# Performance work log

Hardware: AMD Instinct MI355X
Metric: run time of the kernel (lower is better)

The kernel has to match this reference:

```python
import jax, jax.numpy as jnp
import numpy as np

B, T, C = 2, 2048, 1024
NH = 16
DFF = 4096
EPS = 1e-5


def setup_inputs() -> dict:
    key = jax.random.key(0)
    ks = jax.random.split(key, 12)
    s = 0.02
    return {
        "x": jax.random.normal(ks[0], (B, T, C), dtype=jnp.float32),
        "Wq": jax.random.normal(ks[1], (C, C), dtype=jnp.float32) * s,
        "bq": jax.random.normal(ks[2], (C,), dtype=jnp.float32) * s,
        "Wk": jax.random.normal(ks[3], (C, C), dtype=jnp.float32) * s,
        "bk": jax.random.normal(ks[4], (C,), dtype=jnp.float32) * s,
        "Wv": jax.random.normal(ks[5], (C, C), dtype=jnp.float32) * s,
        "bv": jax.random.normal(ks[6], (C,), dtype=jnp.float32) * s,
        "W1": jax.random.normal(ks[7], (C, DFF), dtype=jnp.float32) * s,
        "b1": jax.random.normal(ks[8], (DFF,), dtype=jnp.float32) * s,
        "W2": jax.random.normal(ks[9], (DFF, C), dtype=jnp.float32) * s,
        "b2": jax.random.normal(ks[10], (C,), dtype=jnp.float32) * s,
        "ln_w": jnp.ones((C,), dtype=jnp.float32),
    }


def _layernorm(x, w):
    # LayerNorm over last dim, weight only (bias=False), eps=1e-5
    mu = jnp.mean(x, axis=-1, keepdims=True)
    var = jnp.mean(jnp.square(x - mu), axis=-1, keepdims=True)
    return (x - mu) / jnp.sqrt(var + EPS) * w


def reference(x, Wq, bq, Wk, bk, Wv, bv, W1, b1, W2, b2, ln_w):
    Bx, Tx, Cx = x.shape
    hd = Cx // NH
    q = (x @ Wq + bq).reshape(Bx, Tx, NH, hd).transpose(0, 2, 1, 3)  # [B,H,T,hd]
    k = (x @ Wk + bk).reshape(Bx, Tx, NH, hd).transpose(0, 2, 1, 3)
    v = (x @ Wv + bv).reshape(Bx, Tx, NH, hd).transpose(0, 2, 1, 3)
    # NOTE: original scales by sqrt(d_k) = sqrt(FULL model dim C), not head dim
    scores = jnp.einsum("bhqd,bhkd->bhqk", q, k) / jnp.sqrt(jnp.float32(Cx))
    causal = jnp.tril(jnp.ones((Tx, Tx), dtype=bool))
    scores = jnp.where(causal[None, None, :, :], scores, -jnp.inf)
    attn = jax.nn.softmax(scores, axis=-1)
    head_out = jnp.einsum("bhqk,bhkd->bhqd", attn, v)
    a = head_out.transpose(0, 2, 1, 3).reshape(Bx, Tx, Cx)
    # residuals: out = x + ln(x) with SHARED ln weight
    h = a + _layernorm(a, ln_w)
    f = jax.nn.relu(h @ W1 + b1) @ W2 + b2
    out = f + _layernorm(f, ln_w)
    return out
```

## Files before the change

kernel.cpp:

```cpp
#include <hip/hip_runtime.h>
#include <math.h>


typedef __attribute__((ext_vector_type(8))) short short8;
typedef __attribute__((ext_vector_type(4))) float f32x4;

__device__ __forceinline__ unsigned short f2bf(float f) {
    unsigned u = __builtin_bit_cast(unsigned, f);
    unsigned r = u + 0x7fffu + ((u >> 16) & 1u);
    return (unsigned short)(r >> 16);
}

__global__ __launch_bounds__(256) void prep_kernel(
    const float* __restrict__ x,  const float* __restrict__ Wq,
    const float* __restrict__ Wk, const float* __restrict__ Wv,
    const float* __restrict__ W1, const float* __restrict__ W2,
    const float* __restrict__ bq, const float* __restrict__ bk,
    unsigned short* __restrict__ x_bf,  unsigned short* __restrict__ Wqk_t,
    unsigned short* __restrict__ Wvt,   unsigned short* __restrict__ W1t,
    unsigned short* __restrict__ W2t,   float* __restrict__ bqk)
{
    const int bid = blockIdx.x;
    const int tid = threadIdx.x;

    if (bid < 4096) {
        const int i = (bid * 256 + tid) * 4;
        float4 v = *(const float4*)(x + i);
        ushort4 o;
        o.x = f2bf(v.x); o.y = f2bf(v.y); o.z = f2bf(v.z); o.w = f2bf(v.w);
        *(ushort4*)(x_bf + i) = o;
        return;
    }
    if (bid >= 15360) {
        const int i = (bid - 15360) * 256 + tid;
        bqk[i] = i < 1024 ? bq[i] : bk[i - 1024];
        return;
    }

    __shared__ float tile[32][33];
    const float* src; unsigned short* dst; int K, N, t;
    if (bid < 5120)       { t = bid - 4096;  src = Wq; dst = Wqk_t;            K = 1024; N = 1024; }
    else if (bid < 6144)  { t = bid - 5120;  src = Wk; dst = Wqk_t + 1048576;  K = 1024; N = 1024; }
    else if (bid < 7168)  { t = bid - 6144;  src = Wv; dst = Wvt;              K = 1024; N = 1024; }
    else if (bid < 11264) { t = bid - 7168;  src = W1; dst = W1t;              K = 1024; N = 4096; }
    else                  { t = bid - 11264; src = W2; dst = W2t;              K = 4096; N = 1024; }

    const int ncols = N >> 5;
    const int n0 = (t % ncols) * 32;
    const int k0 = (t / ncols) * 32;
    const int tx = tid & 31;
    const int ty = tid >> 5;
#pragma unroll
    for (int i = 0; i < 4; ++i)
        tile[ty + i * 8][tx] = src[(size_t)(k0 + ty + i * 8) * N + n0 + tx];
    __syncthreads();
#pragma unroll
    for (int i = 0; i < 4; ++i)
        dst[(size_t)(n0 + ty + i * 8) * K + k0 + tx] = f2bf(tile[tx][ty + i * 8]);
}

template <int TM, int TN>
__device__ __forceinline__ void gemm_body(
    unsigned short* As, unsigned short* Bs,
    const unsigned short* __restrict__ A, const unsigned short* __restrict__ Bt,
    const float* __restrict__ bias, float* __restrict__ Cf,
    unsigned short* __restrict__ Cb, int M, int N, int K, int mode,
    int bx, int by)
{
    constexpr int NI   = TM / 32;
    constexpr int NJ   = TN / 32;
    constexpr int NPA  = TM / 8;
    constexpr int NPB  = TN / 8;
    constexpr int MAXA = (NPA + 3) / 4;
    constexpr int MAXB = (NPB + 3) / 4;

    const int tid  = threadIdx.x;
    const int lane = tid & 63;
    const int w    = tid >> 6;
    const int wm   = (w & 1) * (TM / 2);
    const int wn   = (w >> 1) * (TN / 2);
    const int fm   = lane & 15;
    const int quad = lane >> 4;

    const int row0 = by * TM;
    const int col0 = bx * TN;

    const int srow = lane >> 3;
    const int scol = ((lane & 7) ^ srow) << 3;

    const unsigned short* aptr[MAXA];
    int aoff[MAXA];
#pragma unroll
    for (int i = 0; i < MAXA; ++i) {
        const int p = w + i * 4;
        if (p < NPA) {
            aptr[i] = A + (size_t)(row0 + p * 8 + srow) * K + scol;
            aoff[i] = p * 8 * 64;
        }
    }
    const unsigned short* bptr[MAXB];
    int boff[MAXB];
#pragma unroll
    for (int i = 0; i < MAXB; ++i) {
        const int p = w + i * 4;
        if (p < NPB) {
            bptr[i] = Bt + (size_t)(col0 + p * 8 + srow) * K + scol;
            boff[i] = p * 8 * 64;
        }
    }

    f32x4 acc[NI][NJ] = {};

    for (int k0 = 0; k0 < K; k0 += 64) {
        __syncthreads();
#pragma unroll
        for (int i = 0; i < MAXA; ++i)
            if (w + i * 4 < NPA)
                __builtin_amdgcn_global_load_lds(
                    (const __attribute__((address_space(1))) void*)(aptr[i] + k0),
                    (__attribute__((address_space(3))) void*)&As[aoff[i]], 16, 0, 0);
#pragma unroll
        for (int i = 0; i < MAXB; ++i)
            if (w + i * 4 < NPB)
                __builtin_amdgcn_global_load_lds(
                    (const __attribute__((address_space(1))) void*)(bptr[i] + k0),
                    (__attribute__((address_space(3))) void*)&Bs[boff[i]], 16, 0, 0);
        __syncthreads();

#pragma unroll
        for (int kh = 0; kh < 2; ++kh) {
            short8 af[NI], bf[NJ];
#pragma unroll
            for (int i = 0; i < NI; ++i) {
                const int r = wm + i * 16 + fm;
                const int sl = ((kh << 2) | quad) ^ (r & 7);
                af[i] = *(const short8*)&As[r * 64 + sl * 8];
            }
#pragma unroll
            for (int j = 0; j < NJ; ++j) {
                const int r = wn + j * 16 + fm;
                const int sl = ((kh << 2) | quad) ^ (r & 7);
                bf[j] = *(const short8*)&Bs[r * 64 + sl * 8];
            }
#pragma unroll
            for (int i = 0; i < NI; ++i)
#pragma unroll
                for (int j = 0; j < NJ; ++j)
                    acc[i][j] = __builtin_amdgcn_mfma_f32_16x16x32_bf16(
                        af[i], bf[j], acc[i][j], 0, 0, 0);
        }
    }

#pragma unroll
    for (int j = 0; j < NJ; ++j) {
        const int col = col0 + wn + j * 16 + fm;
        const float bcol = (mode == 3) ? 0.f : bias[col];
#pragma unroll
        for (int i = 0; i < NI; ++i) {
            const int rbase = row0 + wm + i * 16 + quad * 4;
#pragma unroll
            for (int r = 0; r < 4; ++r) {
                const int row = rbase + r;
                float val = acc[i][j][r] + ((mode == 3) ? bias[row] : bcol);
                if (mode == 1) val = fmaxf(val, 0.f);
                if (mode == 0) Cf[(size_t)row * N + col] = val;
                else           Cb[(size_t)row * N + col] = f2bf(val);
            }
        }
    }
}

template <int TM, int TN>
__global__ __launch_bounds__(256) void gemm_bf16_mfma(
    const unsigned short* __restrict__ A, const unsigned short* __restrict__ Bt,
    const float* __restrict__ bias, float* __restrict__ Cf,
    unsigned short* __restrict__ Cb, int M, int N, int K, int mode)
{
    __shared__ unsigned short As[TM * 64];
    __shared__ unsigned short Bs[TN * 64];
    gemm_body<TM, TN>(As, Bs, A, Bt, bias, Cf, Cb, M, N, K, mode,
                      blockIdx.x, blockIdx.y);
}

template <int TM, int TN>
__global__ __launch_bounds__(256) void gemm_xcd(
    const unsigned short* __restrict__ A, const unsigned short* __restrict__ Bt,
    const float* __restrict__ bias, float* __restrict__ Cf,
    unsigned short* __restrict__ Cb, int M, int N, int K, int mode,
    int nx, int rows_per_xcd)
{
    __shared__ unsigned short As[TM * 64];
    __shared__ unsigned short Bs[TN * 64];
    const int xcd = blockIdx.x & 7;
    const int idx = blockIdx.x >> 3;
    const int bx  = idx % nx;
    const int by  = xcd * rows_per_xcd + idx / nx;
    gemm_body<TM, TN>(As, Bs, A, Bt, bias, Cf, Cb, M, N, K, mode, bx, by);
}

template <int TM, int TN>
__global__ __launch_bounds__(256) void gemm_dual(
    const unsigned short* __restrict__ A0, const unsigned short* __restrict__ B0,
    const float* __restrict__ bias0, unsigned short* __restrict__ C0,
    int M0, int N0, int K0, int mode0, int nb0, int nx0,
    const unsigned short* __restrict__ A1, const unsigned short* __restrict__ B1,
    const float* __restrict__ bias1, unsigned short* __restrict__ C1,
    int M1, int N1, int K1, int mode1, int nx1)
{
    __shared__ unsigned short As[TM * 64];
    __shared__ unsigned short Bs[TN * 64];
    const int bid = blockIdx.x;
    if (bid < nb0) {
        gemm_body<TM, TN>(As, Bs, A0, B0, bias0, nullptr, C0,
                          M0, N0, K0, mode0, bid % nx0, bid / nx0);
    } else {
        const int t = bid - nb0;
        gemm_body<TM, TN>(As, Bs, A1, B1, bias1, nullptr, C1,
                          M1, N1, K1, mode1, t % nx1, t / nx1);
    }
}

__global__ __launch_bounds__(256) void fattn_mfma(
    const unsigned short* __restrict__ qk,
    const unsigned short* __restrict__ vt,
    float* __restrict__ a)
{
    const int T = 2048, LDQK = 2048, LDVT = 4096, OUTC = 1024;
    const float cs = 0.04508422f;

    __shared__ unsigned short Qs[64 * 64];
    __shared__ unsigned short Ks[64 * 64];
    __shared__ unsigned short Vs[64 * 64];
    __shared__ unsigned short Ps[4][16][72];

    const int tid  = threadIdx.x;
    const int lane = tid & 63;
    const int w    = tid >> 6;
    const int fm   = lane & 15;
    const int quad = lane >> 4;
    const int srow = lane >> 3;
    const int scol = ((lane & 7) ^ srow) << 3;

    const int n  = blockIdx.x;
    const int lo = n & 255, hi = n >> 8;
    const int h  = ((lo >> 5) & 7) | ((hi & 1) << 3);
    const int b  = hi >> 1;
    const int qv = lo & 31;
    const int u  = ((qv & 1) << 4) | ((qv & 2) << 2) | (qv & 4) |
                   ((qv & 8) >> 2) | ((qv & 16) >> 4);
    const int qb = (hi & 1) ? (31 - u) : u;
    const int q0 = qb * 64;

    const size_t rowbase = (size_t)b * T;

#pragma unroll
    for (int i = 0; i < 2; ++i) {
        const int p = w * 2 + i;
        const unsigned short* src = qk + (rowbase + q0 + p * 8 + srow) * LDQK
                                       + h * 64 + scol;
        __builtin_amdgcn_global_load_lds(
            (const __attribute__((address_space(1))) void*)src,
            (__attribute__((address_space(3))) void*)&Qs[p * 8 * 64], 16, 0, 0);
    }
    __syncthreads();
    const int qr = w * 16 + fm;
    short8 qf0 = *(const short8*)&Qs[qr * 64 + ((quad ^ (qr & 7)) << 3)];
    short8 qf1 = *(const short8*)&Qs[qr * 64 + (((4 | quad) ^ (qr & 7)) << 3)];

    short8 ones;
#pragma unroll
    for (int i = 0; i < 8; ++i) ones[i] = (short)0x3F80;

    f32x4 o[4] = {};
    f32x4 lacc = {};

    const int qglob = q0 + w * 16 + fm;

    for (int jt = 0; jt <= qb; ++jt) {
        const int j0 = jt * 64;
        __syncthreads();
#pragma unroll
        for (int i = 0; i < 4; ++i) {
            const int unit = w * 4 + i;
            if (unit < 8) {
                const unsigned short* ksrc = qk + (rowbase + j0 + unit * 8 + srow) * LDQK
                                                + 1024 + h * 64 + scol;
                __builtin_amdgcn_global_load_lds(
                    (const __attribute__((address_space(1))) void*)ksrc,
                    (__attribute__((address_space(3))) void*)&Ks[unit * 8 * 64], 16, 0, 0);
            } else {
                const int p = unit - 8;
                const unsigned short* vsrc = vt + (size_t)(h * 64 + p * 8 + srow) * LDVT
                                                + rowbase + j0 + scol;
                __builtin_amdgcn_global_load_lds(
                    (const __attribute__((address_space(1))) void*)vsrc,
                    (__attribute__((address_space(3))) void*)&Vs[p * 8 * 64], 16, 0, 0);
            }
        }
        __syncthreads();

        f32x4 s[4];
#pragma unroll
        for (int j = 0; j < 4; ++j) {
            const int r = j * 16 + fm;
            short8 k0 = *(const short8*)&Ks[r * 64 + ((quad ^ (r & 7)) << 3)];
            short8 k1 = *(const short8*)&Ks[r * 64 + (((4 | quad) ^ (r & 7)) << 3)];
            f32x4 acc = {};
            acc = __builtin_amdgcn_mfma_f32_16x16x32_bf16(k0, qf0, acc, 0, 0, 0);
            acc = __builtin_amdgcn_mfma_f32_16x16x32_bf16(k1, qf1, acc, 0, 0, 0);
            s[j] = acc;
        }

        if (jt == qb) {
#pragma unroll
            for (int j = 0; j < 4; ++j) {
                const int kbase = j0 + j * 16 + quad * 4;
#pragma unroll
                for (int r = 0; r < 4; ++r) {
                    const float e = exp2f(s[j][r] * cs);
                    s[j][r] = (kbase + r > qglob) ? 0.f : e;
                }
            }
        } else {
#pragma unroll
            for (int j = 0; j < 4; ++j)
#pragma unroll
                for (int r = 0; r < 4; ++r)
                    s[j][r] = exp2f(s[j][r] * cs);
        }

#pragma unroll
        for (int j = 0; j < 4; ++j) {
            const unsigned d0 = (unsigned)f2bf(s[j][0]) | ((unsigned)f2bf(s[j][1]) << 16);
            const unsigned d1 = (unsigned)f2bf(s[j][2]) | ((unsigned)f2bf(s[j][3]) << 16);
            *(uint2*)&Ps[w][fm][j * 16 + quad * 4] = make_uint2(d0, d1);
        }
        short8 pf0 = *(const short8*)&Ps[w][fm][quad * 8];
        short8 pf1 = *(const short8*)&Ps[w][fm][32 + quad * 8];

#pragma unroll
        for (int jd = 0; jd < 4; ++jd) {
            const int r = jd * 16 + fm;
            short8 v0 = *(const short8*)&Vs[r * 64 + ((quad ^ (r & 7)) << 3)];
            short8 v1 = *(const short8*)&Vs[r * 64 + (((4 | quad) ^ (r & 7)) << 3)];
            o[jd] = __builtin_amdgcn_mfma_f32_16x16x32_bf16(pf0, v0, o[jd], 0, 0, 0);
            o[jd] = __builtin_amdgcn_mfma_f32_16x16x32_bf16(pf1, v1, o[jd], 0, 0, 0);
        }
        lacc = __builtin_amdgcn_mfma_f32_16x16x32_bf16(pf0, ones, lacc, 0, 0, 0);
        lacc = __builtin_amdgcn_mfma_f32_16x16x32_bf16(pf1, ones, lacc, 0, 0, 0);
    }

    const size_t orow = rowbase + q0 + w * 16 + quad * 4;
#pragma unroll
    for (int r = 0; r < 4; ++r) {
        const float inv = 1.0f / lacc[r];
#pragma unroll
        for (int jd = 0; jd < 4; ++jd)
            a[(orow + r) * OUTC + h * 64 + jd * 16 + fm] = o[jd][r] * inv;
    }
}

__global__ __launch_bounds__(256) void add_ln_kernel(
    const float* __restrict__ in, const float* __restrict__ w,
    float* __restrict__ outf, unsigned short* __restrict__ outb, int bf16_out)
{
    const int C = 1024;
    const int row = blockIdx.x;
    const int tid = threadIdx.x;
    const int lane = tid & 63;
    const int wv   = tid >> 6;

    __shared__ float red[8];

    float4 xv = *(const float4*)(in + (size_t)row * C + tid * 4);

    float s = xv.x + xv.y + xv.z + xv.w;
#pragma unroll
    for (int o = 32; o > 0; o >>= 1) s += __shfl_xor(s, o, 64);
    if (lane == 0) red[wv] = s;
    __syncthreads();
    const float mu = (red[0] + red[1] + red[2] + red[3]) * (1.0f / 1024.0f);

    float dx = xv.x - mu, dy = xv.y - mu, dz = xv.z - mu, dw = xv.w - mu;
    float v = dx * dx + dy * dy + dz * dz + dw * dw;
#pragma unroll
    for (int o = 32; o > 0; o >>= 1) v += __shfl_xor(v, o, 64);
    if (lane == 0) red[4 + wv] = v;
    __syncthreads();
    const float rstd = rsqrtf((red[4] + red[5] + red[6] + red[7]) * (1.0f / 1024.0f)
                              + 1e-5f);

    float4 wvv = *(const float4*)(w + tid * 4);
    float ox = xv.x + dx * rstd * wvv.x;
    float oy = xv.y + dy * rstd * wvv.y;
    float oz = xv.z + dz * rstd * wvv.z;
    float ow = xv.w + dw * rstd * wvv.w;
    if (bf16_out) {
        ushort4 o4;
        o4.x = f2bf(ox); o4.y = f2bf(oy); o4.z = f2bf(oz); o4.w = f2bf(ow);
        *(ushort4*)(outb + (size_t)row * C + tid * 4) = o4;
    } else {
        *(float4*)(outf + (size_t)row * C + tid * 4) = make_float4(ox, oy, oz, ow);
    }
}

extern "C" void kernel_launch(void* const* d_in, const int* in_sizes, int n_in,
                              void* d_out, int out_size, void* d_ws, size_t ws_size,
                              hipStream_t stream)
{
    const float* x    = (const float*)d_in[0];
    const float* Wq   = (const float*)d_in[1];
    const float* bq   = (const float*)d_in[2];
    const float* Wk   = (const float*)d_in[3];
    const float* bk   = (const float*)d_in[4];
    const float* Wv   = (const float*)d_in[5];
    const float* bv   = (const float*)d_in[6];
    const float* W1   = (const float*)d_in[7];
    const float* b1   = (const float*)d_in[8];
    const float* W2   = (const float*)d_in[9];
    const float* b2   = (const float*)d_in[10];
    const float* ln_w = (const float*)d_in[11];
    float* out = (float*)d_out;
    char* ws = (char*)d_ws;

    const int B = 2, T = 2048, C = 1024, DFF = 4096;
    const int M = B * T;
    const size_t MB = 1048576;

    unsigned short* qk_bf = (unsigned short*)(ws);
    unsigned short* vt_bf = (unsigned short*)(ws + 16 * MB);
    float*          a     = (float*)(ws + 24 * MB);
    unsigned short* x_bf  = (unsigned short*)(ws + 40 * MB);
    unsigned short* Wqk_t = (unsigned short*)(ws + 48 * MB);
    unsigned short* Wvt   = (unsigned short*)(ws + 52 * MB);
    unsigned short* W1t   = (unsigned short*)(ws + 54 * MB);
    unsigned short* W2t   = (unsigned short*)(ws + 62 * MB);
    float*          bqk   = (float*)(ws + 70 * MB);
    unsigned short* u_bf  = (unsigned short*)(ws + 71 * MB);
    unsigned short* h_bf  = x_bf;
    float*          f     = (float*)(ws);

    dim3 blk(256);

    prep_kernel<<<dim3(15368), blk, 0, stream>>>(
        x, Wq, Wk, Wv, W1, W2, bq, bk,
        x_bf, Wqk_t, Wvt, W1t, W2t, bqk);

    gemm_dual<64, 128><<<dim3(1536), blk, 0, stream>>>(
        x_bf, Wqk_t, bqk, qk_bf, M, 2 * C, C, 2, 1024, 16,
        Wvt, x_bf, bv, vt_bf, C, M, C, 3, 32);

    fattn_mfma<<<dim3(1024), blk, 0, stream>>>(qk_bf, vt_bf, a);

    add_ln_kernel<<<dim3(M), blk, 0, stream>>>(a, ln_w, nullptr, h_bf, 1);

    gemm_bf16_mfma<64, 128><<<dim3(DFF / 128, M / 64), blk, 0, stream>>>(
        h_bf, W1t, b1, nullptr, u_bf, M, DFF, C, 1);

    gemm_xcd<128, 64><<<dim3(512), blk, 0, stream>>>(
        u_bf, W2t, b2, f, nullptr, M, C, DFF, 0, 16, 4);

    add_ln_kernel<<<dim3(M), blk, 0, stream>>>(f, ln_w, out, nullptr, 0);
}
```

Before: 316.1 us.

## Split-K the W2 GEMM into two halves and widen prep transpose tiles

The second FFN GEMM (K=4096) now launches 1024 blocks, each computing half the K range. One half writes with bias into f and the other writes a raw partial into the old attention buffer. The final add+LayerNorm kernel sums the two partials as it loads them. This doubles parallelism for a GEMM that previously had only 512 blocks, at the cost of an extra fp32 M×C write and read. Separately, the weight transpose/convert prep kernel uses 64×64 tiles with float4 loads and ushort4 stores, cutting block count and making memory accesses wider.

```diff
diff --git a/kernel.cpp b/kernel.cpp
--- a/kernel.cpp
+++ b/kernel.cpp
@@ -31,32 +31,45 @@
         *(ushort4*)(x_bf + i) = o;
         return;
     }
-    if (bid >= 15360) {
-        const int i = (bid - 15360) * 256 + tid;
+    if (bid >= 6912) {
+        const int i = (bid - 6912) * 256 + tid;
         bqk[i] = i < 1024 ? bq[i] : bk[i - 1024];
         return;
     }
 
-    __shared__ float tile[32][33];
+    __shared__ float tile[64][65];
     const float* src; unsigned short* dst; int K, N, t;
-    if (bid < 5120)       { t = bid - 4096;  src = Wq; dst = Wqk_t;            K = 1024; N = 1024; }
-    else if (bid < 6144)  { t = bid - 5120;  src = Wk; dst = Wqk_t + 1048576;  K = 1024; N = 1024; }
-    else if (bid < 7168)  { t = bid - 6144;  src = Wv; dst = Wvt;              K = 1024; N = 1024; }
-    else if (bid < 11264) { t = bid - 7168;  src = W1; dst = W1t;              K = 1024; N = 4096; }
-    else                  { t = bid - 11264; src = W2; dst = W2t;              K = 4096; N = 1024; }
-
-    const int ncols = N >> 5;
-    const int n0 = (t % ncols) * 32;
-    const int k0 = (t / ncols) * 32;
-    const int tx = tid & 31;
-    const int ty = tid >> 5;
-#pragma unroll
-    for (int i = 0; i < 4; ++i)
-        tile[ty + i * 8][tx] = src[(size_t)(k0 + ty + i * 8) * N + n0 + tx];
+    if (bid < 4352)      { t = bid - 4096; src = Wq; dst = Wqk_t;           K = 1024; N = 1024; }
+    else if (bid < 4608) { t = bid - 4352; src = Wk; dst = Wqk_t + 1048576; K = 1024; N = 1024; }
+    else if (bid < 4864) { t = bid - 4608; src = Wv; dst = Wvt;             K = 1024; N = 1024; }
+    else if (bid < 5888) { t = bid - 4864; src = W1; dst = W1t;             K = 1024; N = 4096; }
+    else                 { t = bid - 5888; src = W2; dst = W2t;             K = 4096; N = 1024; }
+
+    const int ncols = N >> 6;
+    const int n0 = (t % ncols) * 64;
+    const int k0 = (t / ncols) * 64;
+    const int tx = tid & 15;
+    const int ty = tid >> 4;
+#pragma unroll
+    for (int i = 0; i < 4; ++i) {
+        const int r = ty + i * 16;
+        float4 v = *(const float4*)(src + (size_t)(k0 + r) * N + n0 + tx * 4);
+        tile[r][tx * 4 + 0] = v.x;
+        tile[r][tx * 4 + 1] = v.y;
+        tile[r][tx * 4 + 2] = v.z;
+        tile[r][tx * 4 + 3] = v.w;
+    }
     __syncthreads();
 #pragma unroll
-    for (int i = 0; i < 4; ++i)
-        dst[(size_t)(n0 + ty + i * 8) * K + k0 + tx] = f2bf(tile[tx][ty + i * 8]);
+    for (int i = 0; i < 4; ++i) {
+        const int n = ty + i * 16;
+        ushort4 o;
+        o.x = f2bf(tile[tx * 4 + 0][n]);
+        o.y = f2bf(tile[tx * 4 + 1][n]);
+        o.z = f2bf(tile[tx * 4 + 2][n]);
+        o.w = f2bf(tile[tx * 4 + 3][n]);
+        *(ushort4*)(dst + (size_t)(n0 + n) * K + k0 + tx * 4) = o;
+    }
 }
 
 template <int TM, int TN>
@@ -65,7 +78,7 @@
     const unsigned short* __restrict__ A, const unsigned short* __restrict__ Bt,
     const float* __restrict__ bias, float* __restrict__ Cf,
     unsigned short* __restrict__ Cb, int M, int N, int K, int mode,
-    int bx, int by)
+    int bx, int by, int kbeg, int kend)
 {
     constexpr int NI   = TM / 32;
     constexpr int NJ   = TN / 32;
@@ -111,7 +124,7 @@
 
     f32x4 acc[NI][NJ] = {};
 
-    for (int k0 = 0; k0 < K; k0 += 64) {
+    for (int k0 = kbeg; k0 < kend; k0 += 64) {
         __syncthreads();
 #pragma unroll
         for (int i = 0; i < MAXA; ++i)
@@ -154,7 +167,7 @@
 #pragma unroll
     for (int j = 0; j < NJ; ++j) {
         const int col = col0 + wn + j * 16 + fm;
-        const float bcol = (mode == 3) ? 0.f : bias[col];
+        const float bcol = (mode == 3 || mode == 4) ? 0.f : bias[col];
 #pragma unroll
         for (int i = 0; i < NI; ++i) {
             const int rbase = row0 + wm + i * 16 + quad * 4;
@@ -163,8 +176,8 @@
                 const int row = rbase + r;
                 float val = acc[i][j][r] + ((mode == 3) ? bias[row] : bcol);
                 if (mode == 1) val = fmaxf(val, 0.f);
-                if (mode == 0) Cf[(size_t)row * N + col] = val;
-                else           Cb[(size_t)row * N + col] = f2bf(val);
+                if (mode == 0 || mode == 4) Cf[(size_t)row * N + col] = val;
+                else                        Cb[(size_t)row * N + col] = f2bf(val);
             }
         }
     }
@@ -179,23 +192,27 @@
     __shared__ unsigned short As[TM * 64];
     __shared__ unsigned short Bs[TN * 64];
     gemm_body<TM, TN>(As, Bs, A, Bt, bias, Cf, Cb, M, N, K, mode,
-                      blockIdx.x, blockIdx.y);
+                      blockIdx.x, blockIdx.y, 0, K);
 }
 
 template <int TM, int TN>
-__global__ __launch_bounds__(256) void gemm_xcd(
+__global__ __launch_bounds__(256) void gemm_splitk(
     const unsigned short* __restrict__ A, const unsigned short* __restrict__ Bt,
-    const float* __restrict__ bias, float* __restrict__ Cf,
-    unsigned short* __restrict__ Cb, int M, int N, int K, int mode,
-    int nx, int rows_per_xcd)
+    const float* __restrict__ bias, float* __restrict__ C0,
+    float* __restrict__ C1, int M, int N, int K,
+    int nxh, int rows_per_xcd_h, int nbh)
 {
     __shared__ unsigned short As[TM * 64];
     __shared__ unsigned short Bs[TN * 64];
-    const int xcd = blockIdx.x & 7;
-    const int idx = blockIdx.x >> 3;
-    const int bx  = idx % nx;
-    const int by  = xcd * rows_per_xcd + idx / nx;
-    gemm_body<TM, TN>(As, Bs, A, Bt, bias, Cf, Cb, M, N, K, mode, bx, by);
+    const int half = blockIdx.x >= nbh;
+    const int r    = blockIdx.x - (half ? nbh : 0);
+    const int xcd  = blockIdx.x & 7;
+    const int idx  = r >> 3;
+    const int bx   = idx % nxh;
+    const int by   = xcd * rows_per_xcd_h + idx / nxh;
+    const int kb   = half ? (K >> 1) : 0;
+    gemm_body<TM, TN>(As, Bs, A, Bt, bias, half ? C1 : C0, nullptr,
+                      M, N, K, half ? 4 : 0, bx, by, kb, kb + (K >> 1));
 }
 
 template <int TM, int TN>
@@ -212,11 +229,11 @@
     const int bid = blockIdx.x;
     if (bid < nb0) {
         gemm_body<TM, TN>(As, Bs, A0, B0, bias0, nullptr, C0,
-                          M0, N0, K0, mode0, bid % nx0, bid / nx0);
+                          M0, N0, K0, mode0, bid % nx0, bid / nx0, 0, K0);
     } else {
         const int t = bid - nb0;
         gemm_body<TM, TN>(As, Bs, A1, B1, bias1, nullptr, C1,
-                          M1, N1, K1, mode1, t % nx1, t / nx1);
+                          M1, N1, K1, mode1, t % nx1, t / nx1, 0, K1);
     }
 }
 
@@ -361,7 +378,8 @@
 }
 
 __global__ __launch_bounds__(256) void add_ln_kernel(
-    const float* __restrict__ in, const float* __restrict__ w,
+    const float* __restrict__ in, const float* __restrict__ in2,
+    const float* __restrict__ w,
     float* __restrict__ outf, unsigned short* __restrict__ outb, int bf16_out)
 {
     const int C = 1024;
@@ -373,6 +391,10 @@
     __shared__ float red[8];
 
     float4 xv = *(const float4*)(in + (size_t)row * C + tid * 4);
+    if (in2) {
+        float4 yv = *(const float4*)(in2 + (size_t)row * C + tid * 4);
+        xv.x += yv.x; xv.y += yv.y; xv.z += yv.z; xv.w += yv.w;
+    }
 
     float s = xv.x + xv.y + xv.z + xv.w;
 #pragma unroll
@@ -439,10 +461,11 @@
     unsigned short* u_bf  = (unsigned short*)(ws + 71 * MB);
     unsigned short* h_bf  = x_bf;
     float*          f     = (float*)(ws);
+    float*          f2    = a;
 
     dim3 blk(256);
 
-    prep_kernel<<<dim3(15368), blk, 0, stream>>>(
+    prep_kernel<<<dim3(6920), blk, 0, stream>>>(
         x, Wq, Wk, Wv, W1, W2, bq, bk,
         x_bf, Wqk_t, Wvt, W1t, W2t, bqk);
 
@@ -452,13 +475,13 @@
 
     fattn_mfma<<<dim3(1024), blk, 0, stream>>>(qk_bf, vt_bf, a);
 
-    add_ln_kernel<<<dim3(M), blk, 0, stream>>>(a, ln_w, nullptr, h_bf, 1);
+    add_ln_kernel<<<dim3(M), blk, 0, stream>>>(a, nullptr, ln_w, nullptr, h_bf, 1);
 
     gemm_bf16_mfma<64, 128><<<dim3(DFF / 128, M / 64), blk, 0, stream>>>(
         h_bf, W1t, b1, nullptr, u_bf, M, DFF, C, 1);
 
-    gemm_xcd<128, 64><<<dim3(512), blk, 0, stream>>>(
-        u_bf, W2t, b2, f, nullptr, M, C, DFF, 0, 16, 4);
-
-    add_ln_kernel<<<dim3(M), blk, 0, stream>>>(f, ln_w, out, nullptr, 0);
-}
+    gemm_splitk<128, 64><<<dim3(1024), blk, 0, stream>>>(
+        u_bf, W2t, b2, f, f2, M, C, DFF, 16, 4, 512);
+
+    add_ln_kernel<<<dim3(M), blk, 0, stream>>>(f, f2, ln_w, out, nullptr, 0);
+}
```

Result: no change. 321.8 us (+1.8%).
